# Performance work log

Measured on AMD Instinct MI355X. Metric: run time of the kernel, lower is better.

The kernel has to match this reference:

```python
import jax, jax.numpy as jnp
import numpy as np
from jax import lax

N_NODES = 10000
N_EDGES = 320000


def setup_inputs() -> dict:
    key = jax.random.key(0)
    ks = jax.random.split(key, 11)
    s = 0.1  # weight init scale
    return {
        "x": jax.random.normal(ks[0], (N_NODES, 4), jnp.float32),
        "edge_index": jax.random.randint(ks[1], (2, N_EDGES), 0, N_NODES, dtype=jnp.int64),
        "edge_weight": jax.random.uniform(ks[2], (N_EDGES,), jnp.float32),
        "W1": s * jax.random.normal(ks[3], (120, 4, 64), jnp.float32),
        "b1": s * jax.random.normal(ks[4], (64,), jnp.float32),
        "W2": s * jax.random.normal(ks[5], (120, 64, 60), jnp.float32),
        "b2": s * jax.random.normal(ks[6], (60,), jnp.float32),
        "W3": s * jax.random.normal(ks[7], (20, 60, 30), jnp.float32),
        "b3": s * jax.random.normal(ks[8], (30,), jnp.float32),
        "W4": s * jax.random.normal(ks[9], (1, 30, 1), jnp.float32),
    }


def _propagate(h, src, dst, norm, n):
    # out[i] = sum_{e:(src_e -> i)} norm_e * h[src_e]   (PyG message+sum aggregate)
    return jax.ops.segment_sum(norm[:, None] * h[src], dst, num_segments=n)


def _cheb_conv(h, src, dst, norm, W, b, n):
    # PyG ChebConv: out = sum_k T_k(L_hat) h @ W_k (+ b), T_0=I, T_1=L_hat,
    # T_k = 2 L_hat T_{k-1} - T_{k-2}. W has shape [K, in, out].
    K = W.shape[0]
    out = h @ W[0]
    if K > 1:
        Tx1 = _propagate(h, src, dst, norm, n)
        out = out + Tx1 @ W[1]
        if K > 2:
            def step(carry, Wk):
                Tx0, Tx1, acc = carry
                Tx2 = 2.0 * _propagate(Tx1, src, dst, norm, n) - Tx0
                return (Tx1, Tx2, acc + Tx2 @ Wk), None
            (_, _, out), _ = lax.scan(step, (h, Tx1, out), W[2:])
    if b is not None:
        out = out + b
    return out


def reference(x, edge_index, edge_weight, W1, b1, W2, b2, W3, b3, W4):
    n = x.shape[0]
    src, dst = edge_index[0], edge_index[1]
    # Scaled Laplacian edge weights with lambda_max=2, sym norm, no self-loops:
    # L_hat = (2/lambda_max) * (I - D^{-1/2} A D^{-1/2}) - I = -D^{-1/2} A D^{-1/2}
    deg = jax.ops.segment_sum(edge_weight, src, num_segments=n)
    dis = jnp.where(deg > 0, deg ** -0.5, 0.0)
    norm = -dis[src] * edge_weight * dis[dst]
    h = jax.nn.silu(_cheb_conv(x, src, dst, norm, W1, b1, n))
    h = jax.nn.silu(_cheb_conv(h, src, dst, norm, W2, b2, n))
    h = jax.nn.silu(_cheb_conv(h, src, dst, norm, W3, b3, n))
    h = _cheb_conv(h, src, dst, norm, W4, None, n)
    return jax.nn.sigmoid(h)
```

## Files before the change

kernel.cpp:

```cpp
#include <hip/hip_runtime.h>
#include <math.h>

#define N_NODES 10000
#define N_EDGES 320000


__global__ void k_init(float* deg, int* cnt, int* fill, int n) {
    int i = blockIdx.x * blockDim.x + threadIdx.x;
    if (i < n) { deg[i] = 0.f; cnt[i] = 0; fill[i] = 0; }
}

__global__ void k_deg(const int* __restrict__ ei, const float* __restrict__ w,
                      float* deg, int E) {
    int e = blockIdx.x * blockDim.x + threadIdx.x;
    if (e < E) atomicAdd(&deg[ei[e]], w[e]);
}

__global__ void k_dis(float* deg, int n) {
    int i = blockIdx.x * blockDim.x + threadIdx.x;
    if (i < n) {
        float d = deg[i];
        deg[i] = (d > 0.f) ? (float)(1.0 / sqrt((double)d)) : 0.f;
    }
}

__global__ void k_norm(const int* __restrict__ ei, const float* __restrict__ w,
                       const float* __restrict__ dis, float* __restrict__ normw,
                       int* cnt, int E) {
    int e = blockIdx.x * blockDim.x + threadIdx.x;
    if (e < E) {
        int s = ei[e], d = ei[E + e];
        normw[e] = -dis[s] * w[e] * dis[d];
        atomicAdd(&cnt[d], 1);
    }
}

__global__ void k_scan(const int* __restrict__ cnt, int* __restrict__ rowptr, int n) {
    __shared__ int part[1024];
    const int PER = 10;
    int t = threadIdx.x;
    int base = t * PER;
    int local[PER];
    int s = 0;
    for (int j = 0; j < PER; j++) {
        int idx = base + j;
        int v = (idx < n) ? cnt[idx] : 0;
        local[j] = v; s += v;
    }
    part[t] = s;
    __syncthreads();
    for (int off = 1; off < 1024; off <<= 1) {
        int v = part[t];
        int u = (t >= off) ? part[t - off] : 0;
        __syncthreads();
        part[t] = v + u;
        __syncthreads();
    }
    int excl = (t > 0) ? part[t - 1] : 0;
    for (int j = 0; j < PER; j++) {
        int idx = base + j;
        if (idx < n) rowptr[idx] = excl;
        excl += local[j];
    }
    if (t == 1023) rowptr[n] = part[1023];
}

__global__ void k_fill(const int* __restrict__ ei, const float* __restrict__ normw,
                       const int* __restrict__ rowptr, int* fill,
                       int2* __restrict__ pr, int E) {
    int e = blockIdx.x * blockDim.x + threadIdx.x;
    if (e < E) {
        int d = ei[E + e];
        int pos = atomicAdd(&fill[d], 1);
        int idx = rowptr[d] + pos;
        pr[idx] = make_int2(ei[e] << 8, __float_as_int(normw[e]));
    }
}

__device__ __forceinline__ float gather_w(const char* __restrict__ tb,
                                          const int2* __restrict__ pr,
                                          int rb, int dg, int lane4) {
    float agg = 0.f;
    int e = 0;
    for (; e + 8 <= dg; e += 8) {
        int2 p[8]; float v[8];
#pragma unroll
        for (int u = 0; u < 8; u++) p[u] = pr[rb + e + u];
#pragma unroll
        for (int u = 0; u < 8; u++)
            v[u] = *(const float*)(tb + (unsigned)p[u].x + lane4);
#pragma unroll
        for (int u = 0; u < 8; u++)
            agg = fmaf(__int_as_float(p[u].y), v[u], agg);
    }
    if (e < dg) {
        int2 p[8]; float v[8];
#pragma unroll
        for (int u = 0; u < 8; u++) p[u] = pr[(e + u < dg) ? (rb + e + u) : rb];
#pragma unroll
        for (int u = 0; u < 8; u++)
            v[u] = *(const float*)(tb + (unsigned)p[u].x + lane4);
#pragma unroll
        for (int u = 0; u < 8; u++) {
            float w = (e + u < dg) ? __int_as_float(p[u].y) : 0.f;
            agg = fmaf(w, v[u], agg);
        }
    }
    return agg;
}

__device__ __forceinline__ float gather_n(const char* __restrict__ tb,
                                          const int2* __restrict__ pr,
                                          int rb, int dg, int lc4, int eo) {
    float agg = 0.f;
    int e = eo;
    for (; e + 32 <= dg; e += 32) {
        int2 p0 = pr[rb + e];
        int2 p1 = pr[rb + e + 16];
        float v0 = *(const float*)(tb + ((unsigned)p0.x >> 4) + lc4);
        float v1 = *(const float*)(tb + ((unsigned)p1.x >> 4) + lc4);
        agg = fmaf(__int_as_float(p0.y), v0, agg);
        agg = fmaf(__int_as_float(p1.y), v1, agg);
    }
    for (; e < dg; e += 16) {
        int2 p = pr[rb + e];
        agg = fmaf(__int_as_float(p.y),
                   *(const float*)(tb + ((unsigned)p.x >> 4) + lc4), agg);
    }
    agg += __shfl_xor(agg, 4);
    agg += __shfl_xor(agg, 8);
    agg += __shfl_xor(agg, 16);
    agg += __shfl_xor(agg, 32);
    return agg;
}

template <int CI, int CO>
__device__ __forceinline__ void dense(float& acc, float t2v,
                                      const float* __restrict__ Wk, int lane) {
#pragma unroll
    for (int c = 0; c < CI; c++) {
        float tb = __int_as_float(__builtin_amdgcn_readlane(__float_as_int(t2v), c));
        float wv;
        if (CO < 64) wv = (lane < CO) ? Wk[c * CO + lane] : 0.f;
        else         wv = Wk[c * CO + lane];
        acc = fmaf(tb, wv, acc);
    }
}


template <int CI, int CO, int MODE, int LAST>
__global__ __launch_bounds__(256) void k_wide(
    const int* __restrict__ rowptr, const int2* __restrict__ pr,
    const float* __restrict__ hin,
    const float* __restrict__ t0, const float* __restrict__ t1,
    float* __restrict__ t2, float* __restrict__ accb,
    const float* __restrict__ Wk, const float* __restrict__ bias,
    const float* __restrict__ W4, float* __restrict__ outp)
{
    int tid = threadIdx.x;
    int lane = tid & 63;
    int node = blockIdx.x * 4 + (tid >> 6);
    int rb = rowptr[node];
    int dg = rowptr[node + 1] - rb;
    int lane4 = lane * 4;

    float acc, t2v;
    if (MODE == 1) {
        float hr = hin[node * 64 + lane];
        acc = (lane < CO) ? bias[lane] : 0.f;
        dense<CI, CO>(acc, hr, Wk, lane);
        t2v = gather_w((const char*)hin, pr, rb, dg, lane4);
        dense<CI, CO>(acc, t2v, Wk + CI * CO, lane);
    } else {
        acc = accb[node * 64 + lane];
        float t0r = t0[node * 64 + lane];
        float agg = gather_w((const char*)t1, pr, rb, dg, lane4);
        t2v = fmaf(2.f, agg, -t0r);
        dense<CI, CO>(acc, t2v, Wk, lane);
    }

    if (LAST == 0) {
        accb[node * 64 + lane] = acc;
        t2[node * 64 + lane] = t2v;
    } else if (LAST == 1) {
        outp[node * 64 + lane] = acc / (1.f + expf(-acc));
    } else {
        float h = acc / (1.f + expf(-acc));
        float w4 = (lane < 30) ? W4[lane] : 0.f;
        float p = h * w4;
        p += __shfl_xor(p, 1);
        p += __shfl_xor(p, 2);
        p += __shfl_xor(p, 4);
        p += __shfl_xor(p, 8);
        p += __shfl_xor(p, 16);
        p += __shfl_xor(p, 32);
        if (lane == 0) outp[node] = 1.f / (1.f + expf(-p));
    }
}

template <int MODE, int LAST>
__global__ __launch_bounds__(256) void k_narrow(
    const int* __restrict__ rowptr, const int2* __restrict__ pr,
    const float* __restrict__ xin,
    const float* __restrict__ t0, const float* __restrict__ t1,
    float* __restrict__ t2, float* __restrict__ accb,
    const float* __restrict__ Wk, const float* __restrict__ bias,
    float* __restrict__ outp)
{
    int tid = threadIdx.x;
    int lane = tid & 63;
    int node = blockIdx.x * 4 + (tid >> 6);
    int rb = rowptr[node];
    int dg = rowptr[node + 1] - rb;
    int lc = lane & 3, eo = lane >> 2, lc4 = lc * 4;

    float acc, t2v;
    if (MODE == 1) {
        float xr = xin[node * 4 + lc];
        acc = bias[lane];
        dense<4, 64>(acc, xr, Wk, lane);
        t2v = gather_n((const char*)xin, pr, rb, dg, lc4, eo);
        dense<4, 64>(acc, t2v, Wk + 4 * 64, lane);
    } else {
        acc = accb[node * 64 + lane];
        float t0r = t0[node * 4 + lc];
        float agg = gather_n((const char*)t1, pr, rb, dg, lc4, eo);
        t2v = fmaf(2.f, agg, -t0r);
        dense<4, 64>(acc, t2v, Wk, lane);
    }

    if (LAST == 0) {
        accb[node * 64 + lane] = acc;
        if (lane < 4) t2[node * 4 + lane] = t2v;
    } else {
        outp[node * 64 + lane] = acc / (1.f + expf(-acc));
    }
}


extern "C" void kernel_launch(void* const* d_in, const int* in_sizes, int n_in,
                              void* d_out, int out_size, void* d_ws, size_t ws_size,
                              hipStream_t stream) {
    const float* x  = (const float*)d_in[0];
    const int*   ei = (const int*)d_in[1];
    const float* ew = (const float*)d_in[2];
    const float* W1 = (const float*)d_in[3];
    const float* b1 = (const float*)d_in[4];
    const float* W2 = (const float*)d_in[5];
    const float* b2 = (const float*)d_in[6];
    const float* W3 = (const float*)d_in[7];
    const float* b3 = (const float*)d_in[8];
    const float* W4 = (const float*)d_in[9];
    float* out = (float*)d_out;

    const int n = N_NODES, E = N_EDGES;

    char* ws = (char*)d_ws;
    size_t off = 0;
    auto alloc = [&](size_t bytes) -> void* {
        void* p = ws + off;
        off += (bytes + 255) & ~(size_t)255;
        return p;
    };
    float* deg    = (float*)alloc(n * 4);
    int*   cnt    = (int*)alloc(n * 4);
    int*   fill   = (int*)alloc(n * 4);
    int*   rowptr = (int*)alloc((n + 4) * 4);
    float* normw  = (float*)alloc((size_t)E * 4);
    int2*  pr     = (int2*)alloc((size_t)E * 8);
    float* t4a  = (float*)alloc(n * 4 * 4);
    float* t4b  = (float*)alloc(n * 4 * 4);
    float* t4c  = (float*)alloc(n * 4 * 4);
    float* tba  = (float*)alloc(n * 64 * 4);
    float* tbb  = (float*)alloc(n * 64 * 4);
    float* tbc  = (float*)alloc(n * 64 * 4);
    float* accb = (float*)alloc(n * 64 * 4);
    float* h1   = (float*)alloc(n * 64 * 4);
    float* h2   = (float*)alloc(n * 64 * 4);
    (void)ws_size; (void)n_in; (void)in_sizes; (void)out_size;

    k_init<<<(n + 255) / 256, 256, 0, stream>>>(deg, cnt, fill, n);
    k_deg <<<(E + 255) / 256, 256, 0, stream>>>(ei, ew, deg, E);
    k_dis <<<(n + 255) / 256, 256, 0, stream>>>(deg, n);
    k_norm<<<(E + 255) / 256, 256, 0, stream>>>(ei, ew, deg, normw, cnt, E);
    k_scan<<<1, 1024, 0, stream>>>(cnt, rowptr, n);
    k_fill<<<(E + 255) / 256, 256, 0, stream>>>(ei, normw, rowptr, fill, pr, E);

    const int G = n / 4;

    {
        const int K = 120;
        float* tb[3] = {t4a, t4b, t4c};
        k_narrow<1, 0><<<G, 256, 0, stream>>>(rowptr, pr, x, nullptr, nullptr,
                                              tb[1], accb, W1, b1, nullptr);
        for (int k = 2; k < K; k++) {
            const float* t0p = (k == 2) ? x : tb[(k - 2) % 3];
            const float* t1p = tb[(k - 1) % 3];
            const float* Wk = W1 + (size_t)k * 4 * 64;
            if (k < K - 1)
                k_narrow<2, 0><<<G, 256, 0, stream>>>(rowptr, pr, nullptr, t0p, t1p,
                                                      tb[k % 3], accb, Wk, nullptr, nullptr);
            else
                k_narrow<2, 1><<<G, 256, 0, stream>>>(rowptr, pr, nullptr, t0p, t1p,
                                                      nullptr, accb, Wk, nullptr, h1);
        }
    }

    {
        const int K = 120;
        float* tb[3] = {tba, tbb, tbc};
        k_wide<64, 60, 1, 0><<<G, 256, 0, stream>>>(rowptr, pr, h1, nullptr, nullptr,
                                                    tb[1], accb, W2, b2, nullptr, nullptr);
        for (int k = 2; k < K; k++) {
            const float* t0p = (k == 2) ? h1 : tb[(k - 2) % 3];
            const float* t1p = tb[(k - 1) % 3];
            const float* Wk = W2 + (size_t)k * 64 * 60;
            if (k < K - 1)
                k_wide<64, 60, 2, 0><<<G, 256, 0, stream>>>(rowptr, pr, nullptr, t0p, t1p,
                                                            tb[k % 3], accb, Wk, nullptr,
                                                            nullptr, nullptr);
            else
                k_wide<64, 60, 2, 1><<<G, 256, 0, stream>>>(rowptr, pr, nullptr, t0p, t1p,
                                                            nullptr, accb, Wk, nullptr,
                                                            nullptr, h2);
        }
    }

    {
        const int K = 20;
        float* tb[3] = {tba, tbb, tbc};
        k_wide<60, 30, 1, 0><<<G, 256, 0, stream>>>(rowptr, pr, h2, nullptr, nullptr,
                                                    tb[1], accb, W3, b3, nullptr, nullptr);
        for (int k = 2; k < K; k++) {
            const float* t0p = (k == 2) ? h2 : tb[(k - 2) % 3];
            const float* t1p = tb[(k - 1) % 3];
            const float* Wk = W3 + (size_t)k * 60 * 30;
            if (k < K - 1)
                k_wide<60, 30, 2, 0><<<G, 256, 0, stream>>>(rowptr, pr, nullptr, t0p, t1p,
                                                            tb[k % 3], accb, Wk, nullptr,
                                                            nullptr, nullptr);
            else
                k_wide<60, 30, 2, 2><<<G, 256, 0, stream>>>(rowptr, pr, nullptr, t0p, t1p,
                                                            nullptr, accb, Wk, nullptr,
                                                            W4, out);
        }
    }
}
```

Measured before the change: 3.427 ms.

## Process two nodes per wavefront and stage Chebyshev weights in shared memory

Each wavefront now handles two nodes instead of one. The two gathers are interleaved for more memory-level parallelism, and each weight load is reused across both nodes' dense accumulations. Weights for the current order are copied into LDS once per block, and launch bounds set occupancy hints. The grid halves, which adds a block-wide sync and LDS traffic per launch and gives fewer blocks to balance uneven degrees.

```diff
diff --git a/kernel.cpp b/kernel.cpp
--- a/kernel.cpp
+++ b/kernel.cpp
@@ -77,11 +77,10 @@
     }
 }
 
-__device__ __forceinline__ float gather_w(const char* __restrict__ tb,
-                                          const int2* __restrict__ pr,
-                                          int rb, int dg, int lane4) {
-    float agg = 0.f;
-    int e = 0;
+__device__ __forceinline__ float gather_w_from(const char* __restrict__ tb,
+                                               const int2* __restrict__ pr,
+                                               int rb, int e, int dg, int lane4,
+                                               float agg) {
     for (; e + 8 <= dg; e += 8) {
         int2 p[8]; float v[8];
 #pragma unroll
@@ -107,6 +106,32 @@
         }
     }
     return agg;
+}
+
+__device__ __forceinline__ void gather_w2(const char* __restrict__ tb,
+                                          const int2* __restrict__ pr,
+                                          int rb0, int dg0, int rb1, int dg1,
+                                          int lane4, float& o0, float& o1) {
+    float a0 = 0.f, a1 = 0.f;
+    int e0 = 0, e1 = 0;
+    while (e0 + 8 <= dg0 && e1 + 8 <= dg1) {
+        int2 p0[8], p1[8]; float v0[8], v1[8];
+#pragma unroll
+        for (int u = 0; u < 8; u++) { p0[u] = pr[rb0 + e0 + u]; p1[u] = pr[rb1 + e1 + u]; }
+#pragma unroll
+        for (int u = 0; u < 8; u++) {
+            v0[u] = *(const float*)(tb + (unsigned)p0[u].x + lane4);
+            v1[u] = *(const float*)(tb + (unsigned)p1[u].x + lane4);
+        }
+#pragma unroll
+        for (int u = 0; u < 8; u++) {
+            a0 = fmaf(__int_as_float(p0[u].y), v0[u], a0);
+            a1 = fmaf(__int_as_float(p1[u].y), v1[u], a1);
+        }
+        e0 += 8; e1 += 8;
+    }
+    o0 = gather_w_from(tb, pr, rb0, e0, dg0, lane4, a0);
+    o1 = gather_w_from(tb, pr, rb1, e1, dg1, lane4, a1);
 }
 
 __device__ __forceinline__ float gather_n(const char* __restrict__ tb,
@@ -135,21 +160,23 @@
 }
 
 template <int CI, int CO>
-__device__ __forceinline__ void dense(float& acc, float t2v,
-                                      const float* __restrict__ Wk, int lane) {
+__device__ __forceinline__ void dense2(float& a0, float x0, float& a1, float x1,
+                                       const float* sW, int lane) {
 #pragma unroll
     for (int c = 0; c < CI; c++) {
-        float tb = __int_as_float(__builtin_amdgcn_readlane(__float_as_int(t2v), c));
-        float wv;
-        if (CO < 64) wv = (lane < CO) ? Wk[c * CO + lane] : 0.f;
-        else         wv = Wk[c * CO + lane];
-        acc = fmaf(tb, wv, acc);
+        float w;
+        if (CO < 64) w = (lane < CO) ? sW[c * CO + lane] : 0.f;
+        else         w = sW[c * CO + lane];
+        float b0 = __int_as_float(__builtin_amdgcn_readlane(__float_as_int(x0), c));
+        float b1 = __int_as_float(__builtin_amdgcn_readlane(__float_as_int(x1), c));
+        a0 = fmaf(b0, w, a0);
+        a1 = fmaf(b1, w, a1);
     }
 }
 
 
 template <int CI, int CO, int MODE, int LAST>
-__global__ __launch_bounds__(256) void k_wide(
+__global__ __launch_bounds__(256, 6) void k_wide(
     const int* __restrict__ rowptr, const int2* __restrict__ pr,
     const float* __restrict__ hin,
     const float* __restrict__ t0, const float* __restrict__ t1,
@@ -157,49 +184,73 @@
     const float* __restrict__ Wk, const float* __restrict__ bias,
     const float* __restrict__ W4, float* __restrict__ outp)
 {
+    __shared__ float sW[(MODE == 1 ? 2 : 1) * CI * CO];
     int tid = threadIdx.x;
+    const int NW = (MODE == 1 ? 2 : 1) * CI * CO;
+    for (int i = tid; i < NW; i += 256) sW[i] = Wk[i];
+    __syncthreads();
+
     int lane = tid & 63;
-    int node = blockIdx.x * 4 + (tid >> 6);
-    int rb = rowptr[node];
-    int dg = rowptr[node + 1] - rb;
     int lane4 = lane * 4;
-
-    float acc, t2v;
+    int node0 = blockIdx.x * 8 + (tid >> 6) * 2;
+    int node1 = node0 + 1;
+    int rb0 = rowptr[node0], dg0 = rowptr[node0 + 1] - rb0;
+    int rb1 = rowptr[node1], dg1 = rowptr[node1 + 1] - rb1;
+
+    float acc0, acc1, t2v0, t2v1;
     if (MODE == 1) {
-        float hr = hin[node * 64 + lane];
-        acc = (lane < CO) ? bias[lane] : 0.f;
-        dense<CI, CO>(acc, hr, Wk, lane);
-        t2v = gather_w((const char*)hin, pr, rb, dg, lane4);
-        dense<CI, CO>(acc, t2v, Wk + CI * CO, lane);
+        float h0 = hin[node0 * 64 + lane];
+        float h1 = hin[node1 * 64 + lane];
+        float b = (lane < CO) ? bias[lane] : 0.f;
+        acc0 = b; acc1 = b;
+        dense2<CI, CO>(acc0, h0, acc1, h1, sW, lane);
+        gather_w2((const char*)hin, pr, rb0, dg0, rb1, dg1, lane4, t2v0, t2v1);
+        dense2<CI, CO>(acc0, t2v0, acc1, t2v1, sW + CI * CO, lane);
     } else {
-        acc = accb[node * 64 + lane];
-        float t0r = t0[node * 64 + lane];
-        float agg = gather_w((const char*)t1, pr, rb, dg, lane4);
-        t2v = fmaf(2.f, agg, -t0r);
-        dense<CI, CO>(acc, t2v, Wk, lane);
+        acc0 = accb[node0 * 64 + lane];
+        acc1 = accb[node1 * 64 + lane];
+        float t00 = t0[node0 * 64 + lane];
+        float t01 = t0[node1 * 64 + lane];
+        float g0, g1;
+        gather_w2((const char*)t1, pr, rb0, dg0, rb1, dg1, lane4, g0, g1);
+        t2v0 = fmaf(2.f, g0, -t00);
+        t2v1 = fmaf(2.f, g1, -t01);
+        dense2<CI, CO>(acc0, t2v0, acc1, t2v1, sW, lane);
     }
 
     if (LAST == 0) {
-        accb[node * 64 + lane] = acc;
-        t2[node * 64 + lane] = t2v;
+        accb[node0 * 64 + lane] = acc0;
+        accb[node1 * 64 + lane] = acc1;
+        t2[node0 * 64 + lane] = t2v0;
+        t2[node1 * 64 + lane] = t2v1;
     } else if (LAST == 1) {
-        outp[node * 64 + lane] = acc / (1.f + expf(-acc));
+        outp[node0 * 64 + lane] = acc0 / (1.f + expf(-acc0));
+        outp[node1 * 64 + lane] = acc1 / (1.f + expf(-acc1));
     } else {
-        float h = acc / (1.f + expf(-acc));
         float w4 = (lane < 30) ? W4[lane] : 0.f;
-        float p = h * w4;
+        float h0 = acc0 / (1.f + expf(-acc0));
+        float p = h0 * w4;
         p += __shfl_xor(p, 1);
         p += __shfl_xor(p, 2);
         p += __shfl_xor(p, 4);
         p += __shfl_xor(p, 8);
         p += __shfl_xor(p, 16);
         p += __shfl_xor(p, 32);
-        if (lane == 0) outp[node] = 1.f / (1.f + expf(-p));
+        if (lane == 0) outp[node0] = 1.f / (1.f + expf(-p));
+        float h1 = acc1 / (1.f + expf(-acc1));
+        float q = h1 * w4;
+        q += __shfl_xor(q, 1);
+        q += __shfl_xor(q, 2);
+        q += __shfl_xor(q, 4);
+        q += __shfl_xor(q, 8);
+        q += __shfl_xor(q, 16);
+        q += __shfl_xor(q, 32);
+        if (lane == 0) outp[node1] = 1.f / (1.f + expf(-q));
     }
 }
 
 template <int MODE, int LAST>
-__global__ __launch_bounds__(256) void k_narrow(
+__global__ __launch_bounds__(256, 8) void k_narrow(
     const int* __restrict__ rowptr, const int2* __restrict__ pr,
     const float* __restrict__ xin,
     const float* __restrict__ t0, const float* __restrict__ t1,
@@ -207,33 +258,51 @@
     const float* __restrict__ Wk, const float* __restrict__ bias,
     float* __restrict__ outp)
 {
+    __shared__ float sW[(MODE == 1 ? 2 : 1) * 4 * 64];
     int tid = threadIdx.x;
+    const int NW = (MODE == 1 ? 2 : 1) * 4 * 64;
+    for (int i = tid; i < NW; i += 256) sW[i] = Wk[i];
+    __syncthreads();
+
     int lane = tid & 63;
-    int node = blockIdx.x * 4 + (tid >> 6);
-    int rb = rowptr[node];
-    int dg = rowptr[node + 1] - rb;
     int lc = lane & 3, eo = lane >> 2, lc4 = lc * 4;
-
-    float acc, t2v;
+    int node0 = blockIdx.x * 8 + (tid >> 6) * 2;
+    int node1 = node0 + 1;
+    int rb0 = rowptr[node0], dg0 = rowptr[node0 + 1] - rb0;
+    int rb1 = rowptr[node1], dg1 = rowptr[node1 + 1] - rb1;
+
+    float acc0, acc1, t2v0, t2v1;
     if (MODE == 1) {
-        float xr = xin[node * 4 + lc];
-        acc = bias[lane];
-        dense<4, 64>(acc, xr, Wk, lane);
-        t2v = gather_n((const char*)xin, pr, rb, dg, lc4, eo);
-        dense<4, 64>(acc, t2v, Wk + 4 * 64, lane);
+        float x0 = xin[node0 * 4 + lc];
+        float x1 = xin[node1 * 4 + lc];
+        float b = bias[lane];
+        acc0 = b; acc1 = b;
+        dense2<4, 64>(acc0, x0, acc1, x1, sW, lane);
+        t2v0 = gather_n((const char*)xin, pr, rb0, dg0, lc4, eo);
+        t2v1 = gather_n((const char*)xin, pr, rb1, dg1, lc4, eo);
+        dense2<4, 64>(acc0, t2v0, acc1, t2v1, sW + 4 * 64, lane);
     } else {
-        acc = accb[node * 64 + lane];
-        float t0r = t0[node * 4 + lc];
-        float agg = gather_n((const char*)t1, pr, rb, dg, lc4, eo);
-        t2v = fmaf(2.f, agg, -t0r);
-        dense<4, 64>(acc, t2v, Wk, lane);
+        acc0 = accb[node0 * 64 + lane];
+        acc1 = accb[node1 * 64 + lane];
+        float t00 = t0[node0 * 4 + lc];
+        float t01 = t0[node1 * 4 + lc];
+        float g0 = gather_n((const char*)t1, pr, rb0, dg0, lc4, eo);
+        float g1 = gather_n((const char*)t1, pr, rb1, dg1, lc4, eo);
+        t2v0 = fmaf(2.f, g0, -t00);
+        t2v1 = fmaf(2.f, g1, -t01);
+        dense2<4, 64>(acc0, t2v0, acc1, t2v1, sW, lane);
     }
 
     if (LAST == 0) {
-        accb[node * 64 + lane] = acc;
-        if (lane < 4) t2[node * 4 + lane] = t2v;
+        accb[node0 * 64 + lane] = acc0;
+        accb[node1 * 64 + lane] = acc1;
+        if (lane < 4) {
+            t2[node0 * 4 + lane] = t2v0;
+            t2[node1 * 4 + lane] = t2v1;
+        }
     } else {
-        outp[node * 64 + lane] = acc / (1.f + expf(-acc));
+        outp[node0 * 64 + lane] = acc0 / (1.f + expf(-acc0));
+        outp[node1 * 64 + lane] = acc1 / (1.f + expf(-acc1));
     }
 }
 
@@ -286,7 +355,7 @@
     k_scan<<<1, 1024, 0, stream>>>(cnt, rowptr, n);
     k_fill<<<(E + 255) / 256, 256, 0, stream>>>(ei, normw, rowptr, fill, pr, E);
 
-    const int G = n / 4;
+    const int G = n / 8;
 
     {
         const int K = 120;
```

Result: no change. 3.432 ms (+0.1%).
